# Kernel tuning notes

Hardware: AMD Instinct MI355X
Metric: run time of the kernel (lower is better)

The kernel has to match this reference:

```python
import jax, jax.numpy as jnp
import numpy as np

NEG = -9e15
SLOPE = 0.02

def setup_inputs() -> dict:
    key = jax.random.key(0)
    k1, k2, k3, k4 = jax.random.split(key, 4)
    N, IN, OUT = 16384, 128, 64
    x = jax.random.normal(k1, (N, IN), dtype=jnp.float32)
    adj = jax.random.randint(k2, (N, N), 0, 2, dtype=jnp.int32)
    weight = jax.random.normal(k3, (IN, OUT), dtype=jnp.float32) * (1.0 / np.sqrt(IN))
    att_weight = jax.random.normal(k4, (2 * OUT, 1), dtype=jnp.float32) * (1.0 / np.sqrt(2 * OUT))
    return {"x": x, "adj": adj, "weight": weight, "att_weight": att_weight}

def reference(x, adj, weight, att_weight):
    out_feature = weight.shape[1]
    Wh = x @ weight                                   # [N, out]
    f_i = Wh @ att_weight[:out_feature, :]            # [N, 1] source term
    f_j = Wh @ att_weight[out_feature:, :]            # [N, 1] dest term
    e = f_i + f_j.T                                   # [N, N] additive scores
    e = jax.nn.leaky_relu(e, negative_slope=SLOPE)
    att = jnp.where(adj > 0, e, NEG)
    att = jax.nn.softmax(att, axis=1)                 # masked row softmax
    h_prime = att @ Wh                                # [N, out]
    return jax.nn.elu(h_prime)                        # concat=True -> elu
```

## Files before the change

### kernel.cpp

```cpp
#include <hip/hip_runtime.h>
#include <cstdint>
#include <cstddef>

#define GN   16384
#define GIN  128
#define GOUT 64
#define NCH  8
#define LOG2E 1.44269504088896340736f

typedef __attribute__((ext_vector_type(8))) short short8;
typedef __attribute__((ext_vector_type(4))) float f32x4;
typedef __attribute__((ext_vector_type(4))) int   int4v;

__device__ __forceinline__ unsigned short f2bf(float f) {
  unsigned u = __float_as_uint(f);
  return (unsigned short)((u + 0x8000u) >> 16);
}

__device__ __forceinline__ unsigned short f2bf_rne(float f) {
  unsigned u = __float_as_uint(f);
  u += 0x7FFFu + ((u >> 16) & 1u);
  return (unsigned short)(u >> 16);
}

__global__ __launch_bounds__(256) void mask_kernel(
    const int* __restrict__ adj, unsigned char* __restrict__ msk)
{
  const unsigned nb = (unsigned)((size_t)GN * (size_t)GN / 8);
  const unsigned stride = gridDim.x * 256;
  for (unsigned b = blockIdx.x * 256 + threadIdx.x; b < nb; b += stride) {
    const int4v* p = (const int4v*)(adj + (size_t)b * 8);
    int4v x0 = __builtin_nontemporal_load(p);
    int4v x1 = __builtin_nontemporal_load(p + 1);
    unsigned by = (unsigned)(x0.x != 0)
                | ((unsigned)(x0.y != 0) << 1)
                | ((unsigned)(x0.z != 0) << 2)
                | ((unsigned)(x0.w != 0) << 3)
                | ((unsigned)(x1.x != 0) << 4)
                | ((unsigned)(x1.y != 0) << 5)
                | ((unsigned)(x1.z != 0) << 6)
                | ((unsigned)(x1.w != 0) << 7);
    msk[b] = (unsigned char)by;
  }
}

__global__ __launch_bounds__(256) void prep_kernel(
    const float* __restrict__ x, const float* __restrict__ w,
    const float* __restrict__ aw, unsigned short* __restrict__ wpk,
    float* __restrict__ fs2, float* __restrict__ fd2)
{
  __shared__ float ws[GIN * GOUT];
  __shared__ float red[2][64][4];

  const int t = threadIdx.x;
  const int rb = blockIdx.x * 64;

  for (int i = t; i < (GIN * GOUT) / 4; i += 256)
    ((float4*)ws)[i] = ((const float4*)w)[i];
  __syncthreads();

  const int r = t & 63, s = t >> 6;
  const int row = rb + r;
  const float* xr = x + (size_t)row * GIN;

  float acc[16];
#pragma unroll
  for (int d = 0; d < 16; ++d) acc[d] = 0.f;

  for (int kk = 0; kk < GIN; kk += 4) {
    float4 xv = *(const float4*)(xr + kk);
    float xa[4] = {xv.x, xv.y, xv.z, xv.w};
#pragma unroll
    for (int u = 0; u < 4; ++u) {
#pragma unroll
      for (int d = 0; d < 16; ++d)
        acc[d] += xa[u] * ws[(kk + u) * GOUT + s * 16 + d];
    }
  }

  const int jc = row >> 5;
  const int qq = (row & 31) >> 3;
  const int tt = row & 7;
  float psrc = 0.f, pdst = 0.f;
#pragma unroll
  for (int d = 0; d < 16; ++d) {
    const int dg = s * 16 + d;
    psrc += acc[d] * aw[dg];
    pdst += acc[d] * aw[GOUT + dg];
    const int f = dg >> 4, n = dg & 15;
    wpk[(size_t)jc * 4096 + f * 1024 + (qq * 16 + n) * 8 + tt] = f2bf_rne(acc[d]);
  }
  red[0][r][s] = psrc;
  red[1][r][s] = pdst;
  __syncthreads();
  if (s == 0) {
    float a_ = red[0][r][0] + red[0][r][1] + red[0][r][2] + red[0][r][3];
    float b_ = red[1][r][0] + red[1][r][1] + red[1][r][2] + red[1][r][3];
    fs2[row] = a_ * LOG2E;
    fd2[row] = b_ * LOG2E;
  }
}

__global__ __launch_bounds__(256) void gat_main(
    const unsigned* __restrict__ bmw, const unsigned short* __restrict__ wpk,
    const float* __restrict__ fs2, const float* __restrict__ fd2,
    float* __restrict__ nump, float* __restrict__ denp)
{
  const int wave  = blockIdx.x * 4 + (threadIdx.x >> 6);
  const int lane  = threadIdx.x & 63;
  const int strip = wave & 255;
  const int chunk = wave >> 8;
  const int m = lane & 15;
  const int q = lane >> 4;
  const int q8 = q << 3;

  int   row[4];
  float fs[4];
  const unsigned* __restrict__ bmr[4];
#pragma unroll
  for (int g = 0; g < 4; ++g) {
    row[g] = strip * 64 + g * 16 + m;
    fs[g] = fs2[row[g]];
    bmr[g] = bmw + (size_t)row[g] * (GN / 32);
  }

  const int CW = GN / NCH;
  const int j0 = chunk * CW;
  const float4* __restrict__ fdv  = (const float4*)fd2;
  const short8* __restrict__ wpk8 = (const short8*)wpk;

  f32x4 acc[4][4];
  f32x4 accd[4];
#pragma unroll
  for (int g = 0; g < 4; ++g) {
    accd[g] = (f32x4){0.f, 0.f, 0.f, 0.f};
#pragma unroll
    for (int b = 0; b < 4; ++b) acc[g][b] = (f32x4){0.f, 0.f, 0.f, 0.f};
  }

  short8 b_ones;
#pragma unroll
  for (int i = 0; i < 8; ++i) b_ones[i] = (short)0x3F80;

  auto pelem = [&](unsigned byte, int t, float fd, float fsv) -> unsigned short {
    float sv = fsv + fd;
    float lv = fmaxf(sv, 0.02f * sv);
    float pe = __builtin_amdgcn_exp2f(lv);
    pe = (byte & (1u << t)) ? pe : 0.f;
    return f2bf(pe);
  };

  auto mk_af = [&](unsigned byte, float4 fA, float4 fB, float fsv) -> short8 {
    short8 af;
    af[0] = (short)pelem(byte, 0, fA.x, fsv);
    af[1] = (short)pelem(byte, 1, fA.y, fsv);
    af[2] = (short)pelem(byte, 2, fA.z, fsv);
    af[3] = (short)pelem(byte, 3, fA.w, fsv);
    af[4] = (short)pelem(byte, 4, fB.x, fsv);
    af[5] = (short)pelem(byte, 5, fB.y, fsv);
    af[6] = (short)pelem(byte, 6, fB.z, fsv);
    af[7] = (short)pelem(byte, 7, fB.w, fsv);
    return af;
  };

#pragma unroll 1
  for (int j = j0; j < j0 + CW; j += 32) {
    const int i4 = (j >> 2) + (q << 1);
    const int wi = j >> 5;

    unsigned wv[4];
#pragma unroll
    for (int g = 0; g < 4; ++g) wv[g] = bmr[g][wi];

    float4 f0 = fdv[i4];
    float4 f1 = fdv[i4 + 1];

    const short8* wb = wpk8 + (size_t)wi * 512 + lane;
    short8 b0 = wb[0];
    short8 b1 = wb[128];
    short8 b2 = wb[256];
    short8 b3 = wb[384];

#pragma unroll
    for (int g = 0; g < 4; ++g) {
      const unsigned byte = (wv[g] >> q8) & 0xffu;
      short8 af = mk_af(byte, f0, f1, fs[g]);
      acc[g][0] = __builtin_amdgcn_mfma_f32_16x16x32_bf16(af, b0, acc[g][0], 0, 0, 0);
      acc[g][1] = __builtin_amdgcn_mfma_f32_16x16x32_bf16(af, b1, acc[g][1], 0, 0, 0);
      acc[g][2] = __builtin_amdgcn_mfma_f32_16x16x32_bf16(af, b2, acc[g][2], 0, 0, 0);
      acc[g][3] = __builtin_amdgcn_mfma_f32_16x16x32_bf16(af, b3, acc[g][3], 0, 0, 0);
      accd[g]   = __builtin_amdgcn_mfma_f32_16x16x32_bf16(af, b_ones, accd[g], 0, 0, 0);
    }
  }

  float* np = nump + (size_t)chunk * GN * GOUT;
  float* dp = denp + (size_t)chunk * GN;
#pragma unroll
  for (int g = 0; g < 4; ++g) {
    const int orow0 = strip * 64 + g * 16 + q * 4;
#pragma unroll
    for (int r = 0; r < 4; ++r) {
      float* nr = np + (size_t)(orow0 + r) * GOUT + m;
      __builtin_nontemporal_store(acc[g][0][r], nr + 0);
      __builtin_nontemporal_store(acc[g][1][r], nr + 16);
      __builtin_nontemporal_store(acc[g][2][r], nr + 32);
      __builtin_nontemporal_store(acc[g][3][r], nr + 48);
      if (m == 0) dp[orow0 + r] = accd[g][r];
    }
  }
}

__global__ __launch_bounds__(256) void fin_kernel(
    const float* __restrict__ nump, const float* __restrict__ denp,
    float* __restrict__ out)
{
  const int g = blockIdx.x * 256 + threadIdx.x;
  if (g >= GN * GOUT) return;
  const int row = g >> 6;
  float s = 0.f, d = 0.f;
#pragma unroll
  for (int c = 0; c < NCH; ++c) {
    s += nump[(size_t)c * GN * GOUT + g];
    d += denp[(size_t)c * GN + row];
  }
  float v = s / d;
  out[g] = (v > 0.f) ? v : expm1f(v);
}

extern "C" void kernel_launch(void* const* d_in, const int* in_sizes, int n_in,
                              void* d_out, int out_size, void* d_ws, size_t ws_size,
                              hipStream_t stream) {
  const float* x   = (const float*)d_in[0];
  const int*   adj = (const int*)d_in[1];
  const float* w   = (const float*)d_in[2];
  const float* aw  = (const float*)d_in[3];
  float* out = (float*)d_out;

  float* nump = (float*)d_ws;
  float* denp = nump + (size_t)NCH * GN * GOUT;
  float* fs2  = denp + (size_t)NCH * GN;
  float* fd2  = fs2 + GN;
  unsigned short* wpk = (unsigned short*)(fd2 + GN);
  unsigned char* msk = (unsigned char*)(wpk + (size_t)512 * 4096);

  mask_kernel<<<2048, 256, 0, stream>>>(adj, msk);
  prep_kernel<<<GN / 64, 256, 0, stream>>>(x, w, aw, wpk, fs2, fd2);
  gat_main<<<(GN / 64) * NCH / 4, 256, 0, stream>>>((const unsigned*)msk, wpk, fs2, fd2, nump, denp);
  fin_kernel<<<(GN * GOUT) / 256, 256, 0, stream>>>(nump, denp, out);
}
```

Measured before the change: 1.483 ms.

## Halve rows per wave, double column chunks, and software-pipeline mask/fd loads

```diff
diff --git a/kernel.cpp b/kernel.cpp
--- a/kernel.cpp
+++ b/kernel.cpp
@@ -5,7 +5,7 @@
 #define GN   16384
 #define GIN  128
 #define GOUT 64
-#define NCH  8
+#define NCH  16
 #define LOG2E 1.44269504088896340736f
 
 typedef __attribute__((ext_vector_type(8))) short short8;
@@ -101,41 +101,39 @@
   }
 }
 
-__global__ __launch_bounds__(256) void gat_main(
+__global__ __launch_bounds__(256, 4) void gat_main(
     const unsigned* __restrict__ bmw, const unsigned short* __restrict__ wpk,
     const float* __restrict__ fs2, const float* __restrict__ fd2,
     float* __restrict__ nump, float* __restrict__ denp)
 {
   const int wave  = blockIdx.x * 4 + (threadIdx.x >> 6);
   const int lane  = threadIdx.x & 63;
-  const int strip = wave & 255;
-  const int chunk = wave >> 8;
+  const int strip = wave & 511;
+  const int chunk = wave >> 9;
   const int m = lane & 15;
   const int q = lane >> 4;
   const int q8 = q << 3;
 
-  int   row[4];
-  float fs[4];
-  const unsigned* __restrict__ bmr[4];
-#pragma unroll
-  for (int g = 0; g < 4; ++g) {
-    row[g] = strip * 64 + g * 16 + m;
-    fs[g] = fs2[row[g]];
-    bmr[g] = bmw + (size_t)row[g] * (GN / 32);
-  }
+  int   row0 = strip * 32 + m;
+  int   row1 = row0 + 16;
+  float fs0 = fs2[row0];
+  float fs1 = fs2[row1];
+  const unsigned* __restrict__ bmr0 = bmw + (size_t)row0 * (GN / 32);
+  const unsigned* __restrict__ bmr1 = bmw + (size_t)row1 * (GN / 32);
 
   const int CW = GN / NCH;
   const int j0 = chunk * CW;
   const float4* __restrict__ fdv  = (const float4*)fd2;
   const short8* __restrict__ wpk8 = (const short8*)wpk;
 
-  f32x4 acc[4][4];
-  f32x4 accd[4];
-#pragma unroll
-  for (int g = 0; g < 4; ++g) {
-    accd[g] = (f32x4){0.f, 0.f, 0.f, 0.f};
-#pragma unroll
-    for (int b = 0; b < 4; ++b) acc[g][b] = (f32x4){0.f, 0.f, 0.f, 0.f};
+  f32x4 acc0[4], acc1[4];
+  f32x4 accd0, accd1;
+  accd0 = (f32x4){0.f, 0.f, 0.f, 0.f};
+  accd1 = (f32x4){0.f, 0.f, 0.f, 0.f};
+#pragma unroll
+  for (int b = 0; b < 4; ++b) {
+    acc0[b] = (f32x4){0.f, 0.f, 0.f, 0.f};
+    acc1[b] = (f32x4){0.f, 0.f, 0.f, 0.f};
   }
 
   short8 b_ones;
@@ -163,49 +161,81 @@
     return af;
   };
 
-#pragma unroll 1
-  for (int j = j0; j < j0 + CW; j += 32) {
+  auto LOADSTEP = [&](int j, unsigned& w0, unsigned& w1, float4& g0, float4& g1) {
+    const int wi = j >> 5;
     const int i4 = (j >> 2) + (q << 1);
+    w0 = bmr0[wi];
+    w1 = bmr1[wi];
+    g0 = fdv[i4];
+    g1 = fdv[i4 + 1];
+  };
+
+  auto COMPS = [&](int j, unsigned w0, unsigned w1, float4 g0, float4 g1) {
     const int wi = j >> 5;
-
-    unsigned wv[4];
-#pragma unroll
-    for (int g = 0; g < 4; ++g) wv[g] = bmr[g][wi];
-
-    float4 f0 = fdv[i4];
-    float4 f1 = fdv[i4 + 1];
-
     const short8* wb = wpk8 + (size_t)wi * 512 + lane;
     short8 b0 = wb[0];
     short8 b1 = wb[128];
     short8 b2 = wb[256];
     short8 b3 = wb[384];
 
-#pragma unroll
-    for (int g = 0; g < 4; ++g) {
-      const unsigned byte = (wv[g] >> q8) & 0xffu;
-      short8 af = mk_af(byte, f0, f1, fs[g]);
-      acc[g][0] = __builtin_amdgcn_mfma_f32_16x16x32_bf16(af, b0, acc[g][0], 0, 0, 0);
-      acc[g][1] = __builtin_amdgcn_mfma_f32_16x16x32_bf16(af, b1, acc[g][1], 0, 0, 0);
-      acc[g][2] = __builtin_amdgcn_mfma_f32_16x16x32_bf16(af, b2, acc[g][2], 0, 0, 0);
-      acc[g][3] = __builtin_amdgcn_mfma_f32_16x16x32_bf16(af, b3, acc[g][3], 0, 0, 0);
-      accd[g]   = __builtin_amdgcn_mfma_f32_16x16x32_bf16(af, b_ones, accd[g], 0, 0, 0);
-    }
+    {
+      const unsigned byte = (w0 >> q8) & 0xffu;
+      short8 af = mk_af(byte, g0, g1, fs0);
+      acc0[0] = __builtin_amdgcn_mfma_f32_16x16x32_bf16(af, b0, acc0[0], 0, 0, 0);
+      acc0[1] = __builtin_amdgcn_mfma_f32_16x16x32_bf16(af, b1, acc0[1], 0, 0, 0);
+      acc0[2] = __builtin_amdgcn_mfma_f32_16x16x32_bf16(af, b2, acc0[2], 0, 0, 0);
+      acc0[3] = __builtin_amdgcn_mfma_f32_16x16x32_bf16(af, b3, acc0[3], 0, 0, 0);
+      accd0   = __builtin_amdgcn_mfma_f32_16x16x32_bf16(af, b_ones, accd0, 0, 0, 0);
+    }
+    {
+      const unsigned byte = (w1 >> q8) & 0xffu;
+      short8 af = mk_af(byte, g0, g1, fs1);
+      acc1[0] = __builtin_amdgcn_mfma_f32_16x16x32_bf16(af, b0, acc1[0], 0, 0, 0);
+      acc1[1] = __builtin_amdgcn_mfma_f32_16x16x32_bf16(af, b1, acc1[1], 0, 0, 0);
+      acc1[2] = __builtin_amdgcn_mfma_f32_16x16x32_bf16(af, b2, acc1[2], 0, 0, 0);
+      acc1[3] = __builtin_amdgcn_mfma_f32_16x16x32_bf16(af, b3, acc1[3], 0, 0, 0);
+      accd1   = __builtin_amdgcn_mfma_f32_16x16x32_bf16(af, b_ones, accd1, 0, 0, 0);
+    }
+  };
+
+  unsigned wA0, wA1, wB0, wB1;
+  float4 fA0, fA1, fB0, fB1;
+
+  LOADSTEP(j0, wA0, wA1, fA0, fA1);
+#pragma unroll 1
+  for (int j = j0; j < j0 + CW; j += 64) {
+    LOADSTEP(j + 32, wB0, wB1, fB0, fB1);
+    COMPS(j, wA0, wA1, fA0, fA1);
+    int jn = j + 64;
+    jn = (jn < j0 + CW) ? jn : j0;
+    LOADSTEP(jn, wA0, wA1, fA0, fA1);
+    COMPS(j + 32, wB0, wB1, fB0, fB1);
   }
 
   float* np = nump + (size_t)chunk * GN * GOUT;
   float* dp = denp + (size_t)chunk * GN;
-#pragma unroll
-  for (int g = 0; g < 4; ++g) {
-    const int orow0 = strip * 64 + g * 16 + q * 4;
+  {
+    const int orow0 = strip * 32 + q * 4;
 #pragma unroll
     for (int r = 0; r < 4; ++r) {
       float* nr = np + (size_t)(orow0 + r) * GOUT + m;
-      __builtin_nontemporal_store(acc[g][0][r], nr + 0);
-      __builtin_nontemporal_store(acc[g][1][r], nr + 16);
-      __builtin_nontemporal_store(acc[g][2][r], nr + 32);
-      __builtin_nontemporal_store(acc[g][3][r], nr + 48);
-      if (m == 0) dp[orow0 + r] = accd[g][r];
+      __builtin_nontemporal_store(acc0[0][r], nr + 0);
+      __builtin_nontemporal_store(acc0[1][r], nr + 16);
+      __builtin_nontemporal_store(acc0[2][r], nr + 32);
+      __builtin_nontemporal_store(acc0[3][r], nr + 48);
+      if (m == 0) dp[orow0 + r] = accd0[r];
+    }
+  }
+  {
+    const int orow0 = strip * 32 + 16 + q * 4;
+#pragma unroll
+    for (int r = 0; r < 4; ++r) {
+      float* nr = np + (size_t)(orow0 + r) * GOUT + m;
+      __builtin_nontemporal_store(acc1[0][r], nr + 0);
+      __builtin_nontemporal_store(acc1[1][r], nr + 16);
+      __builtin_nontemporal_store(acc1[2][r], nr + 32);
+      __builtin_nontemporal_store(acc1[3][r], nr + 48);
+      if (m == 0) dp[orow0 + r] = accd1[r];
     }
   }
 }
@@ -245,6 +275,6 @@
 
   mask_kernel<<<2048, 256, 0, stream>>>(adj, msk);
   prep_kernel<<<GN / 64, 256, 0, stream>>>(x, w, aw, wpk, fs2, fd2);
-  gat_main<<<(GN / 64) * NCH / 4, 256, 0, stream>>>((const unsigned*)msk, wpk, fs2, fd2, nump, denp);
+  gat_main<<<(GN / 32) * NCH / 4, 256, 0, stream>>>((const unsigned*)msk, wpk, fs2, fd2, nump, denp);
   fin_kernel<<<(GN * GOUT) / 256, 256, 0, stream>>>(nump, denp, out);
 }
```

Result: no change. 1.489 ms (+0.4%).

## Factor leaky-ReLU exp into rank-1 terms to remove per-element exp2

Applied to the files above, without the earlier changes.

```diff
diff --git a/kernel.cpp b/kernel.cpp
--- a/kernel.cpp
+++ b/kernel.cpp
@@ -11,11 +11,6 @@
 typedef __attribute__((ext_vector_type(8))) short short8;
 typedef __attribute__((ext_vector_type(4))) float f32x4;
 typedef __attribute__((ext_vector_type(4))) int   int4v;
-
-__device__ __forceinline__ unsigned short f2bf(float f) {
-  unsigned u = __float_as_uint(f);
-  return (unsigned short)((u + 0x8000u) >> 16);
-}
 
 __device__ __forceinline__ unsigned short f2bf_rne(float f) {
   unsigned u = __float_as_uint(f);
@@ -47,7 +42,9 @@
 __global__ __launch_bounds__(256) void prep_kernel(
     const float* __restrict__ x, const float* __restrict__ w,
     const float* __restrict__ aw, unsigned short* __restrict__ wpk,
-    float* __restrict__ fs2, float* __restrict__ fd2)
+    float* __restrict__ fs2, float* __restrict__ fd2,
+    float* __restrict__ c0, float* __restrict__ c1,
+    unsigned* __restrict__ ddpk)
 {
   __shared__ float ws[GIN * GOUT];
   __shared__ float red[2][64][4];
@@ -96,71 +93,72 @@
   if (s == 0) {
     float a_ = red[0][r][0] + red[0][r][1] + red[0][r][2] + red[0][r][3];
     float b_ = red[1][r][0] + red[1][r][1] + red[1][r][2] + red[1][r][3];
-    fs2[row] = a_ * LOG2E;
-    fd2[row] = b_ * LOG2E;
-  }
-}
-
-__global__ __launch_bounds__(256) void gat_main(
+    float fsv = a_ * LOG2E;
+    float fdv = b_ * LOG2E;
+    fs2[row] = fsv;
+    fd2[row] = fdv;
+    c0[row] = exp2f(fsv);
+    c1[row] = exp2f(0.02f * fsv);
+    float d0 = exp2f(fdv);
+    float d1 = exp2f(0.02f * fdv);
+    ddpk[row] = (unsigned)f2bf_rne(d0) | ((unsigned)f2bf_rne(d1) << 16);
+  }
+}
+
+__global__ __launch_bounds__(256, 2) void gat_main(
     const unsigned* __restrict__ bmw, const unsigned short* __restrict__ wpk,
     const float* __restrict__ fs2, const float* __restrict__ fd2,
+    const float* __restrict__ c0, const float* __restrict__ c1,
+    const unsigned* __restrict__ ddpk,
     float* __restrict__ nump, float* __restrict__ denp)
 {
   const int wave  = blockIdx.x * 4 + (threadIdx.x >> 6);
   const int lane  = threadIdx.x & 63;
-  const int strip = wave & 255;
-  const int chunk = wave >> 8;
+  const int strip = wave & 511;
+  const int chunk = wave >> 9;
   const int m = lane & 15;
   const int q = lane >> 4;
   const int q8 = q << 3;
 
-  int   row[4];
-  float fs[4];
-  const unsigned* __restrict__ bmr[4];
-#pragma unroll
-  for (int g = 0; g < 4; ++g) {
-    row[g] = strip * 64 + g * 16 + m;
-    fs[g] = fs2[row[g]];
-    bmr[g] = bmw + (size_t)row[g] * (GN / 32);
-  }
+  const int row0 = strip * 32 + m;
+  const int row1 = row0 + 16;
+  const float nf0 = -fs2[row0];
+  const float nf1 = -fs2[row1];
+  const unsigned* __restrict__ bmr0 = bmw + (size_t)row0 * (GN / 32);
+  const unsigned* __restrict__ bmr1 = bmw + (size_t)row1 * (GN / 32);
 
   const int CW = GN / NCH;
   const int j0 = chunk * CW;
   const float4* __restrict__ fdv  = (const float4*)fd2;
+  const int4v*  __restrict__ ddv  = (const int4v*)ddpk;
   const short8* __restrict__ wpk8 = (const short8*)wpk;
 
-  f32x4 acc[4][4];
-  f32x4 accd[4];
-#pragma unroll
-  for (int g = 0; g < 4; ++g) {
-    accd[g] = (f32x4){0.f, 0.f, 0.f, 0.f};
-#pragma unroll
-    for (int b = 0; b < 4; ++b) acc[g][b] = (f32x4){0.f, 0.f, 0.f, 0.f};
+  f32x4 accP0[4], accM0[4], accP1[4], accM1[4];
+  f32x4 accPd0, accMd0, accPd1, accMd1;
+  accPd0 = accMd0 = accPd1 = accMd1 = (f32x4){0.f, 0.f, 0.f, 0.f};
+#pragma unroll
+  for (int b = 0; b < 4; ++b) {
+    accP0[b] = accM0[b] = accP1[b] = accM1[b] = (f32x4){0.f, 0.f, 0.f, 0.f};
   }
 
   short8 b_ones;
 #pragma unroll
   for (int i = 0; i < 8; ++i) b_ones[i] = (short)0x3F80;
 
-  auto pelem = [&](unsigned byte, int t, float fd, float fsv) -> unsigned short {
-    float sv = fsv + fd;
-    float lv = fmaxf(sv, 0.02f * sv);
-    float pe = __builtin_amdgcn_exp2f(lv);
-    pe = (byte & (1u << t)) ? pe : 0.f;
-    return f2bf(pe);
-  };
-
-  auto mk_af = [&](unsigned byte, float4 fA, float4 fB, float fsv) -> short8 {
-    short8 af;
-    af[0] = (short)pelem(byte, 0, fA.x, fsv);
-    af[1] = (short)pelem(byte, 1, fA.y, fsv);
-    af[2] = (short)pelem(byte, 2, fA.z, fsv);
-    af[3] = (short)pelem(byte, 3, fA.w, fsv);
-    af[4] = (short)pelem(byte, 4, fB.x, fsv);
-    af[5] = (short)pelem(byte, 5, fB.y, fsv);
-    af[6] = (short)pelem(byte, 6, fB.z, fsv);
-    af[7] = (short)pelem(byte, 7, fB.w, fsv);
-    return af;
+  auto mk2 = [&](unsigned byte, float4 fA, float4 fB, int4v dA, int4v dB,
+                 float nf, short8& afp, short8& afm) {
+    float fe[8] = {fA.x, fA.y, fA.z, fA.w, fB.x, fB.y, fB.z, fB.w};
+    unsigned de[8] = {(unsigned)dA.x, (unsigned)dA.y, (unsigned)dA.z, (unsigned)dA.w,
+                      (unsigned)dB.x, (unsigned)dB.y, (unsigned)dB.z, (unsigned)dB.w};
+#pragma unroll
+    for (int t = 0; t < 8; ++t) {
+      const bool cm = (fe[t] >= nf);
+      const unsigned bmask = (unsigned)(-(int)((byte >> t) & 1u));
+      const unsigned lo = cm ? (de[t] & 0xffffu) : 0u;
+      const unsigned hi = cm ? 0u : (de[t] >> 16);
+      afp[t] = (short)(lo & bmask);
+      afm[t] = (short)(hi & bmask);
+    }
   };
 
 #pragma unroll 1
@@ -168,44 +166,77 @@
     const int i4 = (j >> 2) + (q << 1);
     const int wi = j >> 5;
 
-    unsigned wv[4];
-#pragma unroll
-    for (int g = 0; g < 4; ++g) wv[g] = bmr[g][wi];
-
-    float4 f0 = fdv[i4];
-    float4 f1 = fdv[i4 + 1];
+    const unsigned w0 = bmr0[wi];
+    const unsigned w1 = bmr1[wi];
+    const float4 f0 = fdv[i4];
+    const float4 f1 = fdv[i4 + 1];
+    const int4v d0 = ddv[i4];
+    const int4v d1 = ddv[i4 + 1];
 
     const short8* wb = wpk8 + (size_t)wi * 512 + lane;
-    short8 b0 = wb[0];
-    short8 b1 = wb[128];
-    short8 b2 = wb[256];
-    short8 b3 = wb[384];
-
-#pragma unroll
-    for (int g = 0; g < 4; ++g) {
-      const unsigned byte = (wv[g] >> q8) & 0xffu;
-      short8 af = mk_af(byte, f0, f1, fs[g]);
-      acc[g][0] = __builtin_amdgcn_mfma_f32_16x16x32_bf16(af, b0, acc[g][0], 0, 0, 0);
-      acc[g][1] = __builtin_amdgcn_mfma_f32_16x16x32_bf16(af, b1, acc[g][1], 0, 0, 0);
-      acc[g][2] = __builtin_amdgcn_mfma_f32_16x16x32_bf16(af, b2, acc[g][2], 0, 0, 0);
-      acc[g][3] = __builtin_amdgcn_mfma_f32_16x16x32_bf16(af, b3, acc[g][3], 0, 0, 0);
-      accd[g]   = __builtin_amdgcn_mfma_f32_16x16x32_bf16(af, b_ones, accd[g], 0, 0, 0);
+    const short8 b0 = wb[0];
+    const short8 b1 = wb[128];
+    const short8 b2 = wb[256];
+    const short8 b3 = wb[384];
+
+    {
+      short8 afp, afm;
+      mk2((w0 >> q8) & 0xffu, f0, f1, d0, d1, nf0, afp, afm);
+      accP0[0] = __builtin_amdgcn_mfma_f32_16x16x32_bf16(afp, b0, accP0[0], 0, 0, 0);
+      accP0[1] = __builtin_amdgcn_mfma_f32_16x16x32_bf16(afp, b1, accP0[1], 0, 0, 0);
+      accP0[2] = __builtin_amdgcn_mfma_f32_16x16x32_bf16(afp, b2, accP0[2], 0, 0, 0);
+      accP0[3] = __builtin_amdgcn_mfma_f32_16x16x32_bf16(afp, b3, accP0[3], 0, 0, 0);
+      accPd0   = __builtin_amdgcn_mfma_f32_16x16x32_bf16(afp, b_ones, accPd0, 0, 0, 0);
+      accM0[0] = __builtin_amdgcn_mfma_f32_16x16x32_bf16(afm, b0, accM0[0], 0, 0, 0);
+      accM0[1] = __builtin_amdgcn_mfma_f32_16x16x32_bf16(afm, b1, accM0[1], 0, 0, 0);
+      accM0[2] = __builtin_amdgcn_mfma_f32_16x16x32_bf16(afm, b2, accM0[2], 0, 0, 0);
+      accM0[3] = __builtin_amdgcn_mfma_f32_16x16x32_bf16(afm, b3, accM0[3], 0, 0, 0);
+      accMd0   = __builtin_amdgcn_mfma_f32_16x16x32_bf16(afm, b_ones, accMd0, 0, 0, 0);
+    }
+    {
+      short8 afp, afm;
+      mk2((w1 >> q8) & 0xffu, f0, f1, d0, d1, nf1, afp, afm);
+      accP1[0] = __builtin_amdgcn_mfma_f32_16x16x32_bf16(afp, b0, accP1[0], 0, 0, 0);
+      accP1[1] = __builtin_amdgcn_mfma_f32_16x16x32_bf16(afp, b1, accP1[1], 0, 0, 0);
+      accP1[2] = __builtin_amdgcn_mfma_f32_16x16x32_bf16(afp, b2, accP1[2], 0, 0, 0);
+      accP1[3] = __builtin_amdgcn_mfma_f32_16x16x32_bf16(afp, b3, accP1[3], 0, 0, 0);
+      accPd1   = __builtin_amdgcn_mfma_f32_16x16x32_bf16(afp, b_ones, accPd1, 0, 0, 0);
+      accM1[0] = __builtin_amdgcn_mfma_f32_16x16x32_bf16(afm, b0, accM1[0], 0, 0, 0);
+      accM1[1] = __builtin_amdgcn_mfma_f32_16x16x32_bf16(afm, b1, accM1[1], 0, 0, 0);
+      accM1[2] = __builtin_amdgcn_mfma_f32_16x16x32_bf16(afm, b2, accM1[2], 0, 0, 0);
+      accM1[3] = __builtin_amdgcn_mfma_f32_16x16x32_bf16(afm, b3, accM1[3], 0, 0, 0);
+      accMd1   = __builtin_amdgcn_mfma_f32_16x16x32_bf16(afm, b_ones, accMd1, 0, 0, 0);
     }
   }
 
   float* np = nump + (size_t)chunk * GN * GOUT;
   float* dp = denp + (size_t)chunk * GN;
-#pragma unroll
-  for (int g = 0; g < 4; ++g) {
-    const int orow0 = strip * 64 + g * 16 + q * 4;
+  {
+    const int orow0 = strip * 32 + q * 4;
 #pragma unroll
     for (int r = 0; r < 4; ++r) {
+      const float cp = c0[orow0 + r];
+      const float cm_ = c1[orow0 + r];
       float* nr = np + (size_t)(orow0 + r) * GOUT + m;
-      __builtin_nontemporal_store(acc[g][0][r], nr + 0);
-      __builtin_nontemporal_store(acc[g][1][r], nr + 16);
-      __builtin_nontemporal_store(acc[g][2][r], nr + 32);
-      __builtin_nontemporal_store(acc[g][3][r], nr + 48);
-      if (m == 0) dp[orow0 + r] = accd[g][r];
+      __builtin_nontemporal_store(cp * accP0[0][r] + cm_ * accM0[0][r], nr + 0);
+      __builtin_nontemporal_store(cp * accP0[1][r] + cm_ * accM0[1][r], nr + 16);
+      __builtin_nontemporal_store(cp * accP0[2][r] + cm_ * accM0[2][r], nr + 32);
+      __builtin_nontemporal_store(cp * accP0[3][r] + cm_ * accM0[3][r], nr + 48);
+      if (m == 0) dp[orow0 + r] = cp * accPd0[r] + cm_ * accMd0[r];
+    }
+  }
+  {
+    const int orow0 = strip * 32 + 16 + q * 4;
+#pragma unroll
+    for (int r = 0; r < 4; ++r) {
+      const float cp = c0[orow0 + r];
+      const float cm_ = c1[orow0 + r];
+      float* nr = np + (size_t)(orow0 + r) * GOUT + m;
+      __builtin_nontemporal_store(cp * accP1[0][r] + cm_ * accM1[0][r], nr + 0);
+      __builtin_nontemporal_store(cp * accP1[1][r] + cm_ * accM1[1][r], nr + 16);
+      __builtin_nontemporal_store(cp * accP1[2][r] + cm_ * accM1[2][r], nr + 32);
+      __builtin_nontemporal_store(cp * accP1[3][r] + cm_ * accM1[3][r], nr + 48);
+      if (m == 0) dp[orow0 + r] = cp * accPd1[r] + cm_ * accMd1[r];
     }
   }
 }
@@ -240,11 +271,15 @@
   float* denp = nump + (size_t)NCH * GN * GOUT;
   float* fs2  = denp + (size_t)NCH * GN;
   float* fd2  = fs2 + GN;
-  unsigned short* wpk = (unsigned short*)(fd2 + GN);
+  float* c0   = fd2 + GN;
+  float* c1   = c0 + GN;
+  unsigned* ddpk = (unsigned*)(c1 + GN);
+  unsigned short* wpk = (unsigned short*)(ddpk + GN);
   unsigned char* msk = (unsigned char*)(wpk + (size_t)512 * 4096);
 
   mask_kernel<<<2048, 256, 0, stream>>>(adj, msk);
-  prep_kernel<<<GN / 64, 256, 0, stream>>>(x, w, aw, wpk, fs2, fd2);
-  gat_main<<<(GN / 64) * NCH / 4, 256, 0, stream>>>((const unsigned*)msk, wpk, fs2, fd2, nump, denp);
+  prep_kernel<<<GN / 64, 256, 0, stream>>>(x, w, aw, wpk, fs2, fd2, c0, c1, ddpk);
+  gat_main<<<(GN / 32) * NCH / 4, 256, 0, stream>>>((const unsigned*)msk, wpk,
+                                                    fs2, fd2, c0, c1, ddpk, nump, denp);
   fin_kernel<<<(GN * GOUT) / 256, 256, 0, stream>>>(nump, denp, out);
 }
```

After: 1.523 ms. +2.7%, slower.
